# Performance work log

Hardware: AMD Instinct MI355X
Metric: run time of the kernel (lower is better)

## Reference

```python
import jax, jax.numpy as jnp
import numpy as np

N_NODES = 50000


def gcn_conv(x, W, b, edge_index, n_nodes):
    """torch_geometric GCNConv: linear -> symmetric-normalized scatter-add with self-loops."""
    h = x @ W  # [N, out]
    src = jnp.concatenate([edge_index[0], jnp.arange(n_nodes)])  # add self-loops
    dst = jnp.concatenate([edge_index[1], jnp.arange(n_nodes)])
    deg = jax.ops.segment_sum(jnp.ones_like(dst, dtype=h.dtype), dst, num_segments=n_nodes)
    dinv = jnp.where(deg > 0, jax.lax.rsqrt(deg), 0.0)  # deg^-1/2, inf -> 0
    norm = dinv[src] * dinv[dst]                         # [E+N]
    msg = h[src] * norm[:, None]                         # gather + scale
    out = jax.ops.segment_sum(msg, dst, num_segments=n_nodes)  # scatter-add
    return out + b


def setup_inputs() -> dict:
    key = jax.random.key(0)
    k1, k2, k3, k4, k5, k6 = jax.random.split(key, 6)
    nhid, nfeat = 128, 256
    E = 800000
    x = jax.random.normal(k1, (N_NODES, nhid), dtype=jnp.float32)
    edge_index = jax.random.randint(k2, (2, E), 0, N_NODES, dtype=jnp.int64)
    s1 = 1.0 / np.sqrt(nhid)
    W1 = jax.random.uniform(k3, (nhid, nhid), jnp.float32, -s1, s1)
    b1 = jnp.zeros((nhid,), jnp.float32)
    W2 = jax.random.uniform(k4, (nhid, nfeat), jnp.float32, -s1, s1)
    b2 = jnp.zeros((nfeat,), jnp.float32)
    return {"x": x, "edge_index": edge_index, "W1": W1, "b1": b1, "W2": W2, "b2": b2}


def reference(x, edge_index, W1, b1, W2, b2):
    # eval mode: dropout is identity
    h = jax.nn.relu(gcn_conv(x, W1, b1, edge_index, N_NODES))
    out = jax.nn.relu(gcn_conv(h, W2, b2, edge_index, N_NODES))
    return out
```

## Files before the change

kernel.cpp:

```cpp
#include <hip/hip_runtime.h>


typedef __attribute__((ext_vector_type(8))) _Float16 half8;
typedef __attribute__((ext_vector_type(4))) _Float16 half4v;
typedef __attribute__((ext_vector_type(4))) float floatx4;

#define BSHIFT 7
#define BNODES 128
#define BCAP   4096

__global__ __launch_bounds__(256) void scatter_conv_kernel(const int* __restrict__ src,
                                                           const int* __restrict__ dst,
                                                           int* __restrict__ bucket_fill,
                                                           unsigned* __restrict__ bucketed,
                                                           const float* __restrict__ W1,
                                                           const float* __restrict__ W2,
                                                           _Float16* __restrict__ wt1,
                                                           _Float16* __restrict__ wt2,
                                                           int E, int chunk, int NB) {
    int t = threadIdx.x;
    if (blockIdx.x >= 256) {
        int idx = (blockIdx.x - 256) * 256 + t;
        if (idx < 128 * 128) {
            int nn = idx >> 7, k = idx & 127;
            wt1[idx] = (_Float16)W1[k * 128 + nn];
        } else if (idx < (128 + 256) * 128) {
            int j = idx - 128 * 128;
            int nn = j >> 7, k = j & 127;
            wt2[j] = (_Float16)W2[k * 256 + nn];
        }
        return;
    }
    extern __shared__ int sh[];
    int* hist = sh;
    int* base_loc = sh + NB;
    int* cur2 = sh + 2 * NB;
    for (int i = t; i < NB; i += 256) { hist[i] = 0; cur2[i] = 0; }
    __syncthreads();
    int cbeg = blockIdx.x * chunk;
    int cend = min(E, cbeg + chunk);
    for (int e = cbeg + t; e < cend; e += 256)
        atomicAdd(&hist[dst[e] >> BSHIFT], 1);
    __syncthreads();
    for (int i = t; i < NB; i += 256) {
        int c = hist[i];
        base_loc[i] = c ? atomicAdd(&bucket_fill[i], c) : 0;
    }
    __syncthreads();
    for (int e = cbeg + t; e < cend; e += 256) {
        int d = dst[e];
        int bkt = d >> BSHIFT;
        int r = atomicAdd(&cur2[bkt], 1);
        bucketed[(size_t)bkt * BCAP + base_loc[bkt] + r] =
            (unsigned)src[e] | ((unsigned)(d & (BNODES - 1)) << 16);
    }
}

__global__ __launch_bounds__(256) void build_kernel(const unsigned* __restrict__ bucketed,
                                                    const int* __restrict__ bucket_fill,
                                                    const float* __restrict__ x,
                                                    int* __restrict__ rowstart,
                                                    int* __restrict__ rowend,
                                                    float* __restrict__ dinv,
                                                    int* __restrict__ csr,
                                                    _Float16* __restrict__ xs,
                                                    int N, int NB) {
    __shared__ int deg_loc[BNODES];
    __shared__ int tmp[BNODES];
    __shared__ int cur_loc[BNODES];
    __shared__ float dinv_loc[BNODES];
    int t = threadIdx.x;
    int b = blockIdx.x;
    int n0 = b << BSHIFT;
    int nodes_in = min(BNODES, N - n0);
    size_t wbase = (size_t)b * BCAP;
    int cnt = bucket_fill[b];

    if (t < BNODES) deg_loc[t] = 0;
    __syncthreads();
    for (int e = t; e < cnt; e += 256)
        atomicAdd(&deg_loc[bucketed[wbase + e] >> 16], 1);
    __syncthreads();
    if (t < BNODES) tmp[t] = deg_loc[t];
    __syncthreads();
    for (int off = 1; off < BNODES; off <<= 1) {
        int v = 0;
        if (t < BNODES && t >= off) v = tmp[t - off];
        __syncthreads();
        if (t < BNODES) tmp[t] += v;
        __syncthreads();
    }
    if (t < BNODES) {
        int abs0 = (int)wbase + tmp[t] - deg_loc[t];
        cur_loc[t] = abs0;
        float dv = rsqrtf((float)(deg_loc[t] + 1));
        dinv_loc[t] = dv;
        if (t < nodes_in) {
            rowstart[n0 + t] = abs0;
            rowend[n0 + t] = abs0 + deg_loc[t];
            dinv[n0 + t] = dv;
        }
    }
    __syncthreads();
    for (int e = t; e < cnt; e += 256) {
        unsigned u2 = bucketed[wbase + e];
        int pos = atomicAdd(&cur_loc[u2 >> 16], 1);
        csr[pos] = (int)(u2 & 0xFFFFu);
    }
    int total4 = nodes_in * 32;
    const float4* x4 = (const float4*)(x + (size_t)n0 * 128);
    for (int i = t; i < total4; i += 256) {
        int row = i >> 5;
        float dv = dinv_loc[row];
        float4 v = x4[i];
        half4v h;
        h[0] = (_Float16)(v.x * dv); h[1] = (_Float16)(v.y * dv);
        h[2] = (_Float16)(v.z * dv); h[3] = (_Float16)(v.w * dv);
        *(half4v*)(xs + (size_t)n0 * 128 + (size_t)i * 4) = h;
    }
}

__global__ __launch_bounds__(256) void agg128_kernel(const _Float16* __restrict__ g,
                                                     const int* __restrict__ rowstart,
                                                     const int* __restrict__ rowend,
                                                     const float* __restrict__ dinv,
                                                     const int* __restrict__ csr,
                                                     _Float16* __restrict__ out, int n) {
    int wid = (blockIdx.x * blockDim.x + threadIdx.x) >> 6;
    int lane = threadIdx.x & 63;
    if (wid >= n) return;
    int q = lane >> 4, l16 = lane & 15;
    int beg = rowstart[wid], end = rowend[wid];

    float a[8] = {0.f, 0.f, 0.f, 0.f, 0.f, 0.f, 0.f, 0.f};
    if (q == 0) {
        half8 v = *(const half8*)(g + (size_t)wid * 128 + l16 * 8);
#pragma unroll
        for (int j = 0; j < 8; j++) a[j] = (float)v[j];
    }
    int e = beg + q;
    for (; e + 12 < end; e += 16) {
        int u0 = csr[e];
        int u1 = csr[e + 4];
        int u2 = csr[e + 8];
        int u3 = csr[e + 12];
        half8 v0 = *(const half8*)(g + (size_t)u0 * 128 + l16 * 8);
        half8 v1 = *(const half8*)(g + (size_t)u1 * 128 + l16 * 8);
        half8 v2 = *(const half8*)(g + (size_t)u2 * 128 + l16 * 8);
        half8 v3 = *(const half8*)(g + (size_t)u3 * 128 + l16 * 8);
#pragma unroll
        for (int j = 0; j < 8; j++)
            a[j] += ((float)v0[j] + (float)v1[j]) + ((float)v2[j] + (float)v3[j]);
    }
    for (; e + 4 < end; e += 8) {
        int u0 = csr[e];
        int u1 = csr[e + 4];
        half8 v0 = *(const half8*)(g + (size_t)u0 * 128 + l16 * 8);
        half8 v1 = *(const half8*)(g + (size_t)u1 * 128 + l16 * 8);
#pragma unroll
        for (int j = 0; j < 8; j++) a[j] += (float)v0[j] + (float)v1[j];
    }
    for (; e < end; e += 4) {
        int u = csr[e];
        half8 v = *(const half8*)(g + (size_t)u * 128 + l16 * 8);
#pragma unroll
        for (int j = 0; j < 8; j++) a[j] += (float)v[j];
    }
#pragma unroll
    for (int j = 0; j < 8; j++) {
        a[j] += __shfl_xor(a[j], 16);
        a[j] += __shfl_xor(a[j], 32);
    }
    if (q == 0) {
        float dv = dinv[wid];
        half8 o;
#pragma unroll
        for (int j = 0; j < 8; j++) o[j] = (_Float16)(a[j] * dv);
        *(half8*)(out + (size_t)wid * 128 + l16 * 8) = o;
    }
}

template <bool HALF_OUT>
__global__ __launch_bounds__(256) void gemm_kernel(const _Float16* __restrict__ A,
                                                   const _Float16* __restrict__ Bt,
                                                   const float* __restrict__ bias,
                                                   const float* __restrict__ dinv,
                                                   void* __restrict__ outp,
                                                   int n, int nout) {
    __shared__ _Float16 As[128][136];
    __shared__ _Float16 Bs[128][136];
    int t = threadIdx.x;
    int row0 = blockIdx.x * 128;
    int col0 = blockIdx.y * 128;

#pragma unroll
    for (int i = 0; i < 8; i++) {
        int c = i * 256 + t;
        int r = c >> 4, seg = c & 15;
        int gr = row0 + r;
        if (gr >= n) gr = n - 1;
        uint4 v = *(const uint4*)(A + (size_t)gr * 128 + seg * 8);
        *(uint4*)(&As[r][seg * 8]) = v;
    }
#pragma unroll
    for (int i = 0; i < 8; i++) {
        int c = i * 256 + t;
        int r = c >> 4, seg = c & 15;
        uint4 v = *(const uint4*)(Bt + (size_t)(col0 + r) * 128 + seg * 8);
        *(uint4*)(&Bs[r][seg * 8]) = v;
    }
    __syncthreads();

    int wid = t >> 6, lane = t & 63;
    int wm = wid >> 1, wn = wid & 1;
    int quad = lane >> 4, l16 = lane & 15;

    floatx4 acc[4][4];
#pragma unroll
    for (int mt = 0; mt < 4; mt++)
#pragma unroll
        for (int nt = 0; nt < 4; nt++) acc[mt][nt] = (floatx4){0.f, 0.f, 0.f, 0.f};

#pragma unroll
    for (int ks = 0; ks < 4; ks++) {
        int k0 = ks * 32 + quad * 8;
        half8 a[4], b[4];
#pragma unroll
        for (int mt = 0; mt < 4; mt++)
            a[mt] = *(const half8*)(&As[wm * 64 + mt * 16 + l16][k0]);
#pragma unroll
        for (int nt = 0; nt < 4; nt++)
            b[nt] = *(const half8*)(&Bs[wn * 64 + nt * 16 + l16][k0]);
#pragma unroll
        for (int mt = 0; mt < 4; mt++)
#pragma unroll
            for (int nt = 0; nt < 4; nt++)
                acc[mt][nt] = __builtin_amdgcn_mfma_f32_16x16x32_f16(a[mt], b[nt], acc[mt][nt], 0, 0, 0);
    }

#pragma unroll
    for (int mt = 0; mt < 4; mt++) {
        int rbase = row0 + wm * 64 + mt * 16 + quad * 4;
#pragma unroll
        for (int reg = 0; reg < 4; reg++) {
            int r = rbase + reg;
            if (r < n) {
                float dv = HALF_OUT ? dinv[r] : 1.f;
#pragma unroll
                for (int nt = 0; nt < 4; nt++) {
                    int cc = col0 + wn * 64 + nt * 16 + l16;
                    float val = fmaxf(acc[mt][nt][reg] + bias[cc], 0.f);
                    if (HALF_OUT)
                        ((_Float16*)outp)[(size_t)r * nout + cc] = (_Float16)(val * dv);
                    else
                        ((float*)outp)[(size_t)r * nout + cc] = val;
                }
            }
        }
    }
}

extern "C" void kernel_launch(void* const* d_in, const int* in_sizes, int n_in,
                              void* d_out, int out_size, void* d_ws, size_t ws_size,
                              hipStream_t stream) {
    const float* x  = (const float*)d_in[0];
    const int*   ei = (const int*)d_in[1];
    const float* W1 = (const float*)d_in[2];
    const float* b1 = (const float*)d_in[3];
    const float* W2 = (const float*)d_in[4];
    const float* b2 = (const float*)d_in[5];
    float* out = (float*)d_out;

    int N = in_sizes[0] / 128;
    int E = in_sizes[1] / 2;
    const int* src = ei;
    const int* dst = ei + E;
    int NB = (N + BNODES - 1) >> BSHIFT;

    char* w = (char*)d_ws;
    size_t off = 0;
    auto alloc = [&](size_t bytes) -> char* {
        char* p = w + off;
        off = (off + bytes + 255) & ~(size_t)255;
        return p;
    };
    int*      bucket_fill = (int*)alloc((size_t)NB * 4);
    unsigned* bucketed    = (unsigned*)alloc((size_t)NB * BCAP * 4);
    int*      rowstart    = (int*)alloc((size_t)N * 4);
    int*      rowend      = (int*)alloc((size_t)N * 4);
    float*    dinv        = (float*)alloc((size_t)N * 4);
    int*      csr         = (int*)alloc((size_t)NB * BCAP * 4);
    _Float16* wt1         = (_Float16*)alloc((size_t)128 * 128 * 2);
    _Float16* wt2         = (_Float16*)alloc((size_t)256 * 128 * 2);
    _Float16* xs          = (_Float16*)alloc((size_t)N * 128 * 2);
    _Float16* q1          = (_Float16*)alloc((size_t)N * 128 * 2);
    _Float16* p2          = (_Float16*)alloc((size_t)N * 128 * 2);
    _Float16* q2          = (_Float16*)alloc((size_t)N * 128 * 2);

    int chunk = (E + 255) / 256;
    size_t lds3 = (size_t)NB * 12;

    hipMemsetAsync(bucket_fill, 0, (size_t)NB * 4, stream);
    hipLaunchKernelGGL(scatter_conv_kernel, dim3(256 + 192), dim3(256), lds3, stream,
                       src, dst, bucket_fill, bucketed, W1, W2, wt1, wt2, E, chunk, NB);
    hipLaunchKernelGGL(build_kernel, dim3(NB), dim3(256), 0, stream,
                       bucketed, bucket_fill, x, rowstart, rowend, dinv, csr, xs, N, NB);

    int gbm = (N + 127) / 128;
    int nb_agg = (N + 3) / 4;
    hipLaunchKernelGGL(agg128_kernel, dim3(nb_agg), dim3(256), 0, stream, xs, rowstart, rowend, dinv, csr, q1, N);
    hipLaunchKernelGGL((gemm_kernel<true>), dim3(gbm, 1), dim3(256), 0, stream, q1, wt1, b1, dinv, (void*)p2, N, 128);
    hipLaunchKernelGGL(agg128_kernel, dim3(nb_agg), dim3(256), 0, stream, p2, rowstart, rowend, dinv, csr, q2, N);
    hipLaunchKernelGGL((gemm_kernel<false>), dim3(gbm, 2), dim3(256), 0, stream, q2, wt2, b2, dinv, (void*)out, N, 256);
}
```

Before: 214.0 us.

## Slice feature aggregation into four column passes for cache locality

The neighbor aggregation kernel is split into four sequential column passes of 32 halves (64 bytes) each. Each wave handles one node and one slice, with 8 lanes per edge and 8 edges in flight. The aim is to shrink the gathered working set per pass so it stays resident in L2/MALL, at the cost of re-reading the CSR indices four times. The index reads are made nontemporal, and each gather is narrowed to 8-byte loads, which may reduce memory efficiency per request.

After: 319.4 us. 49.3% more time.

```diff
diff --git a/kernel.cpp b/kernel.cpp
--- a/kernel.cpp
+++ b/kernel.cpp
@@ -120,63 +120,53 @@
     }
 }
 
-__global__ __launch_bounds__(256) void agg128_kernel(const _Float16* __restrict__ g,
-                                                     const int* __restrict__ rowstart,
-                                                     const int* __restrict__ rowend,
-                                                     const float* __restrict__ dinv,
-                                                     const int* __restrict__ csr,
-                                                     _Float16* __restrict__ out, int n) {
-    int wid = (blockIdx.x * blockDim.x + threadIdx.x) >> 6;
+__global__ __launch_bounds__(256) void agg128_sliced_kernel(const _Float16* __restrict__ g,
+                                                            const int* __restrict__ rowstart,
+                                                            const int* __restrict__ rowend,
+                                                            const float* __restrict__ dinv,
+                                                            const int* __restrict__ csr,
+                                                            _Float16* __restrict__ out,
+                                                            int n, int nb_per_pass) {
+    int pass = blockIdx.x / nb_per_pass;
+    int blk  = blockIdx.x - pass * nb_per_pass;
+    int wid  = blk * 4 + (threadIdx.x >> 6);
     int lane = threadIdx.x & 63;
     if (wid >= n) return;
-    int q = lane >> 4, l16 = lane & 15;
+    int oct = lane >> 3, l8 = lane & 7;
+    const _Float16* gp = g + pass * 32;
+
     int beg = rowstart[wid], end = rowend[wid];
-
-    float a[8] = {0.f, 0.f, 0.f, 0.f, 0.f, 0.f, 0.f, 0.f};
-    if (q == 0) {
-        half8 v = *(const half8*)(g + (size_t)wid * 128 + l16 * 8);
-#pragma unroll
-        for (int j = 0; j < 8; j++) a[j] = (float)v[j];
-    }
-    int e = beg + q;
-    for (; e + 12 < end; e += 16) {
-        int u0 = csr[e];
-        int u1 = csr[e + 4];
-        int u2 = csr[e + 8];
-        int u3 = csr[e + 12];
-        half8 v0 = *(const half8*)(g + (size_t)u0 * 128 + l16 * 8);
-        half8 v1 = *(const half8*)(g + (size_t)u1 * 128 + l16 * 8);
-        half8 v2 = *(const half8*)(g + (size_t)u2 * 128 + l16 * 8);
-        half8 v3 = *(const half8*)(g + (size_t)u3 * 128 + l16 * 8);
-#pragma unroll
-        for (int j = 0; j < 8; j++)
-            a[j] += ((float)v0[j] + (float)v1[j]) + ((float)v2[j] + (float)v3[j]);
-    }
-    for (; e + 4 < end; e += 8) {
-        int u0 = csr[e];
-        int u1 = csr[e + 4];
-        half8 v0 = *(const half8*)(g + (size_t)u0 * 128 + l16 * 8);
-        half8 v1 = *(const half8*)(g + (size_t)u1 * 128 + l16 * 8);
-#pragma unroll
-        for (int j = 0; j < 8; j++) a[j] += (float)v0[j] + (float)v1[j];
-    }
-    for (; e < end; e += 4) {
-        int u = csr[e];
-        half8 v = *(const half8*)(g + (size_t)u * 128 + l16 * 8);
-#pragma unroll
-        for (int j = 0; j < 8; j++) a[j] += (float)v[j];
-    }
-#pragma unroll
-    for (int j = 0; j < 8; j++) {
-        a[j] += __shfl_xor(a[j], 16);
-        a[j] += __shfl_xor(a[j], 32);
-    }
-    if (q == 0) {
+    float a0 = 0.f, a1 = 0.f, a2 = 0.f, a3 = 0.f;
+    if (oct == 0) {
+        half4v s = *(const half4v*)(gp + (size_t)wid * 128 + l8 * 4);
+        a0 = (float)s[0]; a1 = (float)s[1]; a2 = (float)s[2]; a3 = (float)s[3];
+    }
+    int e = beg + oct;
+    for (; e + 8 < end; e += 16) {
+        int u0 = __builtin_nontemporal_load(csr + e);
+        int u1 = __builtin_nontemporal_load(csr + e + 8);
+        half4v v0 = *(const half4v*)(gp + (size_t)u0 * 128 + l8 * 4);
+        half4v v1 = *(const half4v*)(gp + (size_t)u1 * 128 + l8 * 4);
+        a0 += (float)v0[0] + (float)v1[0];
+        a1 += (float)v0[1] + (float)v1[1];
+        a2 += (float)v0[2] + (float)v1[2];
+        a3 += (float)v0[3] + (float)v1[3];
+    }
+    for (; e < end; e += 8) {
+        int u = __builtin_nontemporal_load(csr + e);
+        half4v v = *(const half4v*)(gp + (size_t)u * 128 + l8 * 4);
+        a0 += (float)v[0]; a1 += (float)v[1]; a2 += (float)v[2]; a3 += (float)v[3];
+    }
+    a0 += __shfl_xor(a0, 8);  a0 += __shfl_xor(a0, 16);  a0 += __shfl_xor(a0, 32);
+    a1 += __shfl_xor(a1, 8);  a1 += __shfl_xor(a1, 16);  a1 += __shfl_xor(a1, 32);
+    a2 += __shfl_xor(a2, 8);  a2 += __shfl_xor(a2, 16);  a2 += __shfl_xor(a2, 32);
+    a3 += __shfl_xor(a3, 8);  a3 += __shfl_xor(a3, 16);  a3 += __shfl_xor(a3, 32);
+    if (oct == 0) {
         float dv = dinv[wid];
-        half8 o;
-#pragma unroll
-        for (int j = 0; j < 8; j++) o[j] = (_Float16)(a[j] * dv);
-        *(half8*)(out + (size_t)wid * 128 + l16 * 8) = o;
+        half4v o;
+        o[0] = (_Float16)(a0 * dv); o[1] = (_Float16)(a1 * dv);
+        o[2] = (_Float16)(a2 * dv); o[3] = (_Float16)(a3 * dv);
+        *(half4v*)(out + (size_t)pass * 32 + (size_t)wid * 128 + l8 * 4) = o;
     }
 }
 
@@ -307,9 +297,12 @@
                        bucketed, bucket_fill, x, rowstart, rowend, dinv, csr, xs, N, NB);
 
     int gbm = (N + 127) / 128;
-    int nb_agg = (N + 3) / 4;
-    hipLaunchKernelGGL(agg128_kernel, dim3(nb_agg), dim3(256), 0, stream, xs, rowstart, rowend, dinv, csr, q1, N);
+    int nb_per_pass = (N + 3) / 4;
+    int nb_agg = nb_per_pass * 4;
+    hipLaunchKernelGGL(agg128_sliced_kernel, dim3(nb_agg), dim3(256), 0, stream,
+                       xs, rowstart, rowend, dinv, csr, q1, N, nb_per_pass);
     hipLaunchKernelGGL((gemm_kernel<true>), dim3(gbm, 1), dim3(256), 0, stream, q1, wt1, b1, dinv, (void*)p2, N, 128);
-    hipLaunchKernelGGL(agg128_kernel, dim3(nb_agg), dim3(256), 0, stream, p2, rowstart, rowend, dinv, csr, q2, N);
+    hipLaunchKernelGGL(agg128_sliced_kernel, dim3(nb_agg), dim3(256), 0, stream,
+                       p2, rowstart, rowend, dinv, csr, q2, N, nb_per_pass);
     hipLaunchKernelGGL((gemm_kernel<false>), dim3(gbm, 2), dim3(256), 0, stream, q2, wt2, b2, dinv, (void*)out, N, 256);
 }
```
